# Kernel optimization log

Measured on AMD Instinct MI355X. Metric: run time of the kernel, lower is better.

## Reference

```python
import jax, jax.numpy as jnp
import numpy as np

HID = 1024
NH = 16
HD = HID // NH  # 64


def _lin_params(key, fan_in, fan_out):
    k1, k2 = jax.random.split(key)
    lim = 1.0 / np.sqrt(fan_in)
    W = jax.random.uniform(k1, (fan_in, fan_out), jnp.float32, -lim, lim)
    b = jax.random.uniform(k2, (fan_out,), jnp.float32, -lim, lim)
    return W, b


def setup_inputs() -> dict:
    key = jax.random.key(0)
    ks = jax.random.split(key, 12)
    B, S = 4, 1024
    inp = {
        'query': jax.random.normal(ks[0], (B, S, HID), jnp.float32),
        'key': jax.random.normal(ks[1], (B, S, HID), jnp.float32),
        'value': jax.random.normal(ks[2], (B, S, HID), jnp.float32),
    }
    inp['Wq'], inp['bq'] = _lin_params(ks[3], HID, HID)
    inp['Wk'], inp['bk'] = _lin_params(ks[4], HID, HID)
    inp['Wv'], inp['bv'] = _lin_params(ks[5], HID, HID)
    inp['Wp'], inp['bp'] = _lin_params(ks[6], HID, HID)
    inp['Wup'], inp['bup'] = _lin_params(ks[7], HD, 1)
    inp['Wud'], inp['bud'] = _lin_params(ks[8], HD, 1)
    inp['Wus'], inp['bus'] = _lin_params(ks[9], HID, NH)
    inp['Wo'], inp['bo'] = _lin_params(ks[10], HID, HID)
    return inp


def _split_heads(x, B, S):
    # [B,S,HID] -> [B,NH,S,HD]
    return x.reshape(B, S, NH, HD).transpose(0, 2, 1, 3)


def reference(query, key, value, Wq, bq, Wk, bk, Wv, bv, Wp, bp,
              Wup, bup, Wud, bud, Wus, bus, Wo, bo):
    B, S, _ = query.shape
    len_q = S

    q = query @ Wq + bq   # [B,S,HID]
    k = key @ Wk + bk
    v = value @ Wv + bv

    # Gaussian-window positional bias (per head, per query position)
    p = _split_heads(q @ Wp + bp, B, S)              # [B,NH,S,HD]
    tp = jnp.tanh(p)
    p_i = tp @ Wup + bup                             # [B,NH,S,1]
    z_i = tp @ Wud + bud                             # [B,NH,S,1]
    cen_pos = len_q * jax.nn.sigmoid(p_i)            # [B,NH,S,1]
    win_size = len_q * jax.nn.sigmoid(z_i)           # [B,NH,S,1]
    pos = jnp.arange(len_q, dtype=q.dtype)[None, None, None, :]  # [1,1,1,S]
    bias = (pos - cen_pos) ** 2 / (0.5 * win_size ** 2)          # [B,NH,S,S]

    # per-head alpha gate from raw query
    alpha = jax.nn.sigmoid(query @ Wus + bus)        # [B,S,NH]
    alpha = alpha.reshape(B, S, NH, 1).transpose(0, 2, 1, 3)  # [B,NH,S,1]

    qh = _split_heads(q, B, S)
    kh = _split_heads(k, B, S)
    vh = _split_heads(v, B, S)

    scale = 1.0 / jnp.sqrt(jnp.asarray(HD, q.dtype))
    scores = jnp.einsum('bhqd,bhkd->bhqk', qh, kh) * scale
    scores = scores - alpha * bias                   # inject gated Gaussian bias
    attn = jax.nn.softmax(scores, axis=-1)           # [B,NH,S,S]

    out = jnp.einsum('bhqk,bhkd->bhqd', attn, vh)    # [B,NH,S,HD]
    x = out.transpose(0, 2, 1, 3).reshape(B, S, HID)
    x = x @ Wo + bo
    return x, attn
```

## Files before the change

### kernel.cpp

```cpp
#include <hip/hip_runtime.h>
#include <hip/hip_bf16.h>
#include <math.h>

#define S_LEN 1024
#define HIDN  1024
#define NHEAD 16
#define HDIM  64
#define BATCH 4
#define MTOT  (BATCH * S_LEN)

typedef __attribute__((ext_vector_type(8))) short          bf16v8;
typedef __attribute__((ext_vector_type(8))) unsigned short u16v8;
typedef __attribute__((ext_vector_type(4))) unsigned short u16v4;
typedef __attribute__((ext_vector_type(4))) float          f32v4;

__device__ __forceinline__ unsigned short f2bf_rne(float x) {
    unsigned int u = __float_as_uint(x);
    unsigned int r = (u + 0x7fffu + ((u >> 16) & 1u)) >> 16;
    return (unsigned short)r;
}
__device__ __forceinline__ float bf2f(unsigned short h) {
    return __uint_as_float(((unsigned int)h) << 16);
}
__device__ __forceinline__ void split2(float x, unsigned short& h, unsigned short& l) {
    h = f2bf_rne(x);
    l = f2bf_rne(x - bf2f(h));
}

__global__ __launch_bounds__(256) void split_w4(
    const float* __restrict__ W0, const float* __restrict__ W1,
    const float* __restrict__ W2, const float* __restrict__ W3,
    unsigned short* __restrict__ Hbase, unsigned short* __restrict__ Lbase)
{
    __shared__ float T[64][65];
    const int t  = threadIdx.x;
    const int k0 = blockIdx.y * 64;
    const int n0 = blockIdx.x * 64;
    const int z  = blockIdx.z;
    const float* W = (z == 0) ? W0 : (z == 1) ? W1 : (z == 2) ? W2 : W3;
    unsigned short* H = Hbase + (size_t)z * 1024 * 1024;
    unsigned short* L = Lbase + (size_t)z * 1024 * 1024;

    const int r = t >> 4;
    const int c = (t & 15) * 4;
#pragma unroll
    for (int i = 0; i < 4; ++i) {
        const int rr = r + i * 16;
        const float4 v = *(const float4*)&W[(size_t)(k0 + rr) * 1024 + n0 + c];
        T[rr][c + 0] = v.x; T[rr][c + 1] = v.y;
        T[rr][c + 2] = v.z; T[rr][c + 3] = v.w;
    }
    __syncthreads();

    const int n  = t >> 2;
    const int ko = (t & 3) * 16;
    u16v8 h0, h1, l0, l1;
#pragma unroll
    for (int kk = 0; kk < 8; ++kk) {
        unsigned short hh, ll;
        split2(T[ko + kk][n], hh, ll);
        h0[kk] = hh; l0[kk] = ll;
    }
#pragma unroll
    for (int kk = 0; kk < 8; ++kk) {
        unsigned short hh, ll;
        split2(T[ko + 8 + kk][n], hh, ll);
        h1[kk] = hh; l1[kk] = ll;
    }
    unsigned short* Hp = &H[(size_t)(n0 + n) * 1024 + k0 + ko];
    unsigned short* Lp = &L[(size_t)(n0 + n) * 1024 + k0 + ko];
    *(u16v8*)(Hp)     = h0;
    *(u16v8*)(Hp + 8) = h1;
    *(u16v8*)(Lp)     = l0;
    *(u16v8*)(Lp + 8) = l1;
}

__global__ __launch_bounds__(256) void alpha_kernel(
    const float* __restrict__ X, const float* __restrict__ Wus,
    const float* __restrict__ bus, float* __restrict__ alpha)
{
    __shared__ float Ws[1024 * 16];
    const int t = threadIdx.x;
#pragma unroll
    for (int i = 0; i < 16; ++i) {
        const int idx = t + i * 256;
        *reinterpret_cast<float4*>(&Ws[idx * 4]) =
            *reinterpret_cast<const float4*>(&Wus[idx * 4]);
    }
    __syncthreads();

    const int r = t >> 4, c = t & 15;
    const size_t row = (size_t)blockIdx.x * 16 + r;
    const float* x = &X[row * 1024];
    float acc = 0.f;
    for (int kk = 0; kk < 1024; kk += 4) {
        const float4 xv = *reinterpret_cast<const float4*>(&x[kk]);
        acc = fmaf(xv.x, Ws[(kk + 0) * 16 + c], acc);
        acc = fmaf(xv.y, Ws[(kk + 1) * 16 + c], acc);
        acc = fmaf(xv.z, Ws[(kk + 2) * 16 + c], acc);
        acc = fmaf(xv.w, Ws[(kk + 3) * 16 + c], acc);
    }
    acc += bus[c];
    alpha[row * 16 + c] = 1.f / (1.f + expf(-acc));
}

template<int AF32, int EPI>
__global__ __launch_bounds__(512, 2) void gemm_t(
    const float* __restrict__ Af,
    const unsigned short* __restrict__ Ah, const unsigned short* __restrict__ Al,
    const unsigned short* __restrict__ Bh, const unsigned short* __restrict__ Bl,
    const float* __restrict__ bias, float* __restrict__ Cf,
    unsigned short* __restrict__ Ch, unsigned short* __restrict__ Cl,
    const float* __restrict__ Wup, const float* __restrict__ Wud,
    const float* __restrict__ bup, const float* __restrict__ bud,
    const float* __restrict__ alpha, float* __restrict__ cenp,
    float* __restrict__ c0p)
{
    __shared__ short Ash[128][72];
    __shared__ short Asl[128][72];
    __shared__ short Bsh[64][72];
    __shared__ short Bsl[64][72];
    __shared__ float PSUP[2][128], PSUD[2][128];

    const int t    = threadIdx.x;
    const int bm   = blockIdx.y * 128;
    const int bn   = blockIdx.x * 64;
    const int lane = t & 63;
    const int wid  = t >> 6;
    const int wr   = wid >> 1;
    const int wc   = wid & 1;
    const int fr   = lane & 15;
    const int fq   = lane >> 4;

    f32v4 zero = {0.f, 0.f, 0.f, 0.f};
    f32v4 acc[2][2];
#pragma unroll
    for (int i = 0; i < 2; ++i)
#pragma unroll
        for (int j = 0; j < 2; ++j) acc[i][j] = zero;

    const int sra = t >> 2;
    const int sca = (t & 3) * 16;
    const int tb  = t & 255;
    const int srb = tb >> 2;
    const int scb = (tb & 3) * 16;
    const bool isBl = (t >= 256);
    const unsigned short* pB = isBl ? &Bl[(size_t)(bn + srb) * 1024 + scb]
                                    : &Bh[(size_t)(bn + srb) * 1024 + scb];
    const float* pAf = AF32 ? &Af[(size_t)(bm + sra) * 1024 + sca] : nullptr;
    const unsigned short* pAh = AF32 ? nullptr : &Ah[(size_t)(bm + sra) * 1024 + sca];
    const unsigned short* pAl = AF32 ? nullptr : &Al[(size_t)(bm + sra) * 1024 + sca];

    u16v8 rah0, rah1, ral0, ral1, rb0, rb1;
    auto LOAD = [&](int k0) {
        if (AF32) {
            const float4 a0 = *(const float4*)(pAf + k0);
            const float4 a1 = *(const float4*)(pAf + k0 + 4);
            const float4 a2 = *(const float4*)(pAf + k0 + 8);
            const float4 a3 = *(const float4*)(pAf + k0 + 12);
            const float xs[16] = {a0.x, a0.y, a0.z, a0.w, a1.x, a1.y, a1.z, a1.w,
                                  a2.x, a2.y, a2.z, a2.w, a3.x, a3.y, a3.z, a3.w};
#pragma unroll
            for (int e = 0; e < 8; ++e) {
                unsigned short hh, ll;
                split2(xs[e], hh, ll);
                rah0[e] = hh; ral0[e] = ll;
            }
#pragma unroll
            for (int e = 0; e < 8; ++e) {
                unsigned short hh, ll;
                split2(xs[8 + e], hh, ll);
                rah1[e] = hh; ral1[e] = ll;
            }
        } else {
            rah0 = *(const u16v8*)(pAh + k0);
            rah1 = *(const u16v8*)(pAh + k0 + 8);
            ral0 = *(const u16v8*)(pAl + k0);
            ral1 = *(const u16v8*)(pAl + k0 + 8);
        }
        rb0 = *(const u16v8*)(pB + k0);
        rb1 = *(const u16v8*)(pB + k0 + 8);
    };

    LOAD(0);
    for (int k0 = 0; k0 < 1024; k0 += 64) {
        __syncthreads();
        *(u16v8*)&Ash[sra][sca]     = rah0;
        *(u16v8*)&Ash[sra][sca + 8] = rah1;
        *(u16v8*)&Asl[sra][sca]     = ral0;
        *(u16v8*)&Asl[sra][sca + 8] = ral1;
        if (isBl) {
            *(u16v8*)&Bsl[srb][scb]     = rb0;
            *(u16v8*)&Bsl[srb][scb + 8] = rb1;
        } else {
            *(u16v8*)&Bsh[srb][scb]     = rb0;
            *(u16v8*)&Bsh[srb][scb + 8] = rb1;
        }
        __syncthreads();

        if (k0 + 64 < 1024) LOAD(k0 + 64);

#pragma unroll
        for (int kk2 = 0; kk2 < 2; ++kk2) {
            const int ks = kk2 * 32 + fq * 8;
            bf16v8 fah[2], fal[2], fbh[2], fbl[2];
#pragma unroll
            for (int i = 0; i < 2; ++i) {
                fah[i] = *(const bf16v8*)&Ash[wr * 32 + i * 16 + fr][ks];
                fal[i] = *(const bf16v8*)&Asl[wr * 32 + i * 16 + fr][ks];
            }
#pragma unroll
            for (int j = 0; j < 2; ++j) {
                fbh[j] = *(const bf16v8*)&Bsh[wc * 32 + j * 16 + fr][ks];
                fbl[j] = *(const bf16v8*)&Bsl[wc * 32 + j * 16 + fr][ks];
            }
#pragma unroll
            for (int i = 0; i < 2; ++i)
#pragma unroll
                for (int j = 0; j < 2; ++j) {
                    acc[i][j] = __builtin_amdgcn_mfma_f32_16x16x32_bf16(
                        fah[i], fbh[j], acc[i][j], 0, 0, 0);
                    acc[i][j] = __builtin_amdgcn_mfma_f32_16x16x32_bf16(
                        fah[i], fbl[j], acc[i][j], 0, 0, 0);
                    acc[i][j] = __builtin_amdgcn_mfma_f32_16x16x32_bf16(
                        fal[i], fbh[j], acc[i][j], 0, 0, 0);
                }
        }
    }

    if (EPI == 3) {
        float wupj[2], wudj[2], bb[2];
#pragma unroll
        for (int j = 0; j < 2; ++j) {
            const int colL = wc * 32 + j * 16 + fr;
            wupj[j] = Wup[colL];
            wudj[j] = Wud[colL];
            bb[j]   = bias[bn + colL];
        }
        float su[2][4], sd[2][4];
#pragma unroll
        for (int i = 0; i < 2; ++i)
#pragma unroll
            for (int r = 0; r < 4; ++r) { su[i][r] = 0.f; sd[i][r] = 0.f; }
#pragma unroll
        for (int j = 0; j < 2; ++j)
#pragma unroll
            for (int i = 0; i < 2; ++i)
#pragma unroll
                for (int r = 0; r < 4; ++r) {
                    const float tv = tanhf(acc[i][j][r] + bb[j]);
                    su[i][r] = fmaf(tv, wupj[j], su[i][r]);
                    sd[i][r] = fmaf(tv, wudj[j], sd[i][r]);
                }
#pragma unroll
        for (int i = 0; i < 2; ++i)
#pragma unroll
            for (int r = 0; r < 4; ++r) {
                float a = su[i][r], d = sd[i][r];
                a += __shfl_xor(a, 1); d += __shfl_xor(d, 1);
                a += __shfl_xor(a, 2); d += __shfl_xor(d, 2);
                a += __shfl_xor(a, 4); d += __shfl_xor(d, 4);
                a += __shfl_xor(a, 8); d += __shfl_xor(d, 8);
                if (fr == 0) {
                    const int row = wr * 32 + i * 16 + fq * 4 + r;
                    PSUP[wc][row] = a;
                    PSUD[wc][row] = d;
                }
            }
        __syncthreads();
        if (t < 128) {
            const float ap = PSUP[0][t] + PSUP[1][t] + bup[0];
            const float az = PSUD[0][t] + PSUD[1][t] + bud[0];
            const float cenv = 1024.f / (1.f + expf(-ap));
            const float win  = 1024.f / (1.f + expf(-az));
            const int grow = bm + t;
            const int hd   = bn >> 6;
            const int zz   = (grow >> 10) * 16 + hd;
            const int s    = grow & 1023;
            const float al = alpha[(size_t)grow * 16 + hd];
            cenp[(size_t)zz * 1024 + s] = cenv;
            c0p[(size_t)zz * 1024 + s]  = al * 2.f / (win * win);
        }
        return;
    }

#pragma unroll
    for (int j = 0; j < 2; ++j) {
        const int col = bn + wc * 32 + j * 16 + fr;
        const float bb = bias[col];
#pragma unroll
        for (int i = 0; i < 2; ++i) {
            const int row0 = bm + wr * 32 + i * 16 + fq * 4;
            const f32v4 cv = acc[i][j];
            if (EPI == 2) {
                u16v4 h4, l4;
#pragma unroll
                for (int r = 0; r < 4; ++r) {
                    unsigned short hh, ll;
                    split2(cv[r] + bb, hh, ll);
                    h4[r] = hh; l4[r] = ll;
                }
                const size_t base =
                    ((size_t)((row0 >> 10) * 16 + (col >> 6)) * 64 + (col & 63)) * 1024
                    + (row0 & 1023);
                *(u16v4*)&Ch[base] = h4;
                *(u16v4*)&Cl[base] = l4;
            } else if (EPI == 1) {
#pragma unroll
                for (int r = 0; r < 4; ++r) {
                    unsigned short hh, ll;
                    split2(cv[r] + bb, hh, ll);
                    const size_t idx = (size_t)(row0 + r) * 1024 + col;
                    Ch[idx] = hh; Cl[idx] = ll;
                }
            } else {
#pragma unroll
                for (int r = 0; r < 4; ++r)
                    Cf[(size_t)(row0 + r) * 1024 + col] = cv[r] + bb;
            }
        }
    }
}

#define M0_SHIFT 8.0f
__global__ __launch_bounds__(512, 2) void attn_fused(
    const unsigned short* __restrict__ qh, const unsigned short* __restrict__ ql,
    const unsigned short* __restrict__ kh, const unsigned short* __restrict__ kl,
    const unsigned short* __restrict__ vTh, const unsigned short* __restrict__ vTl,
    const float* __restrict__ cen, const float* __restrict__ c0,
    float* __restrict__ attn,
    unsigned short* __restrict__ oh, unsigned short* __restrict__ ol)
{
    __shared__ unsigned short KH[64][64], KL[64][64];
    __shared__ unsigned short VH[64][64], VL[64][64];
    __shared__ unsigned short PH[128][64], PL[128][64];
    __shared__ float CEN[128], C0S[128];
    __shared__ float LSUM[2][128];
    __shared__ float RINV[128];

    const int bid   = blockIdx.x;
    const int z     = ((bid >> 6) << 3) | (bid & 7);
    const int itile = (bid >> 3) & 7;
    const int i0    = itile * 128;
    const int bq    = z >> 4;
    const int hd    = z & 15;

    const int t    = threadIdx.x;
    const int lane = t & 63;
    const int wid  = t >> 6;
    const int wrp  = wid >> 1;
    const int wc   = wid & 1;
    const int fr   = lane & 15, fq = lane >> 4;

    if (t < 128) {
        CEN[t] = cen[(size_t)z * 1024 + i0 + t];
        C0S[t] = c0[(size_t)z * 1024 + i0 + t];
    }

    bf16v8 qfh_[2][2], qfl_[2][2];
#pragma unroll
    for (int i = 0; i < 2; ++i)
#pragma unroll
        for (int kk = 0; kk < 2; ++kk) {
            const size_t qa = (size_t)(bq * 1024 + i0 + wrp * 32 + i * 16 + fr) * 1024
                              + hd * 64 + kk * 32 + fq * 8;
            qfh_[i][kk] = *(const bf16v8*)&qh[qa];
            qfl_[i][kk] = *(const bf16v8*)&ql[qa];
        }

    float lsum[2][4];
#pragma unroll
    for (int i = 0; i < 2; ++i)
#pragma unroll
        for (int r = 0; r < 4; ++r) lsum[i][r] = 0.f;

    const f32v4 zero = {0.f, 0.f, 0.f, 0.f};

    const int srow = t >> 3;
    const int sseg = t & 7;
    const int ssl  = (sseg ^ (srow & 7)) * 8;
    const unsigned short* vhb = vTh + (size_t)z * 64 * 1024;
    const unsigned short* vlb = vTl + (size_t)z * 64 * 1024;

    u16v8 rkh, rkl, rvh, rvl;
    auto LOADK = [&](int j0) {
        const size_t ga = (size_t)(bq * 1024 + j0 + srow) * 1024 + hd * 64 + sseg * 8;
        rkh = *(const u16v8*)&kh[ga];
        rkl = *(const u16v8*)&kl[ga];
    };
    auto LOADV = [&](int j0) {
        const size_t va = (size_t)srow * 1024 + j0 + sseg * 8;
        rvh = *(const u16v8*)&vhb[va];
        rvl = *(const u16v8*)&vlb[va];
    };

    LOADK(0);
    for (int jt = 0; jt < 16; ++jt) {
        const int j0 = jt * 64;
        unsigned short (*KHc)[64] = (jt & 1) ? VH : KH;
        unsigned short (*KLc)[64] = (jt & 1) ? VL : KL;
        *(u16v8*)&KHc[srow][ssl] = rkh;
        *(u16v8*)&KLc[srow][ssl] = rkl;
        __syncthreads();
        if (jt < 15) LOADK(j0 + 64);

        f32v4 acc[2][2];
#pragma unroll
        for (int i = 0; i < 2; ++i)
#pragma unroll
            for (int j2 = 0; j2 < 2; ++j2) acc[i][j2] = zero;

        __builtin_amdgcn_s_setprio(1);
#pragma unroll
        for (int kk = 0; kk < 2; ++kk) {
            bf16v8 fbh[2], fbl[2];
#pragma unroll
            for (int j2 = 0; j2 < 2; ++j2) {
                const int rb = wc * 32 + j2 * 16 + fr;
                const int sb = ((kk * 4 + fq) ^ (rb & 7)) * 8;
                fbh[j2] = *(const bf16v8*)&KHc[rb][sb];
                fbl[j2] = *(const bf16v8*)&KLc[rb][sb];
            }
#pragma unroll
            for (int i = 0; i < 2; ++i)
#pragma unroll
                for (int j2 = 0; j2 < 2; ++j2) {
                    acc[i][j2] = __builtin_amdgcn_mfma_f32_16x16x32_bf16(
                        qfh_[i][kk], fbh[j2], acc[i][j2], 0, 0, 0);
                    acc[i][j2] = __builtin_amdgcn_mfma_f32_16x16x32_bf16(
                        qfh_[i][kk], fbl[j2], acc[i][j2], 0, 0, 0);
                    acc[i][j2] = __builtin_amdgcn_mfma_f32_16x16x32_bf16(
                        qfl_[i][kk], fbh[j2], acc[i][j2], 0, 0, 0);
                }
        }
        __builtin_amdgcn_s_setprio(0);

#pragma unroll
        for (int i = 0; i < 2; ++i)
#pragma unroll
            for (int r = 0; r < 4; ++r) {
                const int row = wrp * 32 + i * 16 + fq * 4 + r;
                const float cv = CEN[row], cc = C0S[row];
                float al = 0.f;
#pragma unroll
                for (int j2 = 0; j2 < 2; ++j2) {
                    const int col = wc * 32 + j2 * 16 + fr;
                    const float dd = (float)(j0 + col) - cv;
                    const float s  = acc[i][j2][r] * 0.125f - cc * dd * dd;
                    al += __expf(s - M0_SHIFT);
                }
                lsum[i][r] += al;
            }
    }

#pragma unroll
    for (int i = 0; i < 2; ++i)
#pragma unroll
        for (int r = 0; r < 4; ++r) {
            float v = lsum[i][r];
            v += __shfl_xor(v, 1);
            v += __shfl_xor(v, 2);
            v += __shfl_xor(v, 4);
            v += __shfl_xor(v, 8);
            if (fr == 0) LSUM[wc][wrp * 32 + i * 16 + fq * 4 + r] = v;
        }
    __syncthreads();
    if (t < 128) RINV[t] = 1.f / (LSUM[0][t] + LSUM[1][t]);

    f32v4 acco[2][4];
#pragma unroll
    for (int i = 0; i < 2; ++i)
#pragma unroll
        for (int j = 0; j < 4; ++j) acco[i][j] = zero;

    float* attnZ = attn + (size_t)z * 1024 * 1024;

    LOADK(0);
    LOADV(0);
    for (int jt = 0; jt < 16; ++jt) {
        const int j0 = jt * 64;
        __syncthreads();
        *(u16v8*)&KH[srow][ssl] = rkh;
        *(u16v8*)&KL[srow][ssl] = rkl;
        *(u16v8*)&VH[srow][ssl] = rvh;
        *(u16v8*)&VL[srow][ssl] = rvl;
        __syncthreads();
        if (jt < 15) { LOADK(j0 + 64); LOADV(j0 + 64); }

        f32v4 acc[2][2];
#pragma unroll
        for (int i = 0; i < 2; ++i)
#pragma unroll
            for (int j2 = 0; j2 < 2; ++j2) acc[i][j2] = zero;

        __builtin_amdgcn_s_setprio(1);
#pragma unroll
        for (int kk = 0; kk < 2; ++kk) {
            bf16v8 fbh[2], fbl[2];
#pragma unroll
            for (int j2 = 0; j2 < 2; ++j2) {
                const int rb = wc * 32 + j2 * 16 + fr;
                const int sb = ((kk * 4 + fq) ^ (rb & 7)) * 8;
                fbh[j2] = *(const bf16v8*)&KH[rb][sb];
                fbl[j2] = *(const bf16v8*)&KL[rb][sb];
            }
#pragma unroll
            for (int i = 0; i < 2; ++i)
#pragma unroll
                for (int j2 = 0; j2 < 2; ++j2) {
                    acc[i][j2] = __builtin_amdgcn_mfma_f32_16x16x32_bf16(
                        qfh_[i][kk], fbh[j2], acc[i][j2], 0, 0, 0);
                    acc[i][j2] = __builtin_amdgcn_mfma_f32_16x16x32_bf16(
                        qfh_[i][kk], fbl[j2], acc[i][j2], 0, 0, 0);
                    acc[i][j2] = __builtin_amdgcn_mfma_f32_16x16x32_bf16(
                        qfl_[i][kk], fbh[j2], acc[i][j2], 0, 0, 0);
                }
        }
        __builtin_amdgcn_s_setprio(0);

#pragma unroll
        for (int i = 0; i < 2; ++i)
#pragma unroll
            for (int r = 0; r < 4; ++r) {
                const int row = wrp * 32 + i * 16 + fq * 4 + r;
                const float cv = CEN[row], cc = C0S[row], ri = RINV[row];
#pragma unroll
                for (int j2 = 0; j2 < 2; ++j2) {
                    const int col = wc * 32 + j2 * 16 + fr;
                    const float dd = (float)(j0 + col) - cv;
                    const float s  = acc[i][j2][r] * 0.125f - cc * dd * dd;
                    const float p  = __expf(s - M0_SHIFT) * ri;
                    attnZ[(size_t)(i0 + row) * 1024 + j0 + col] = p;
                    unsigned short hv, lv;
                    split2(p, hv, lv);
                    const int slot = ((col >> 3) ^ (row & 7)) * 8 + (col & 7);
                    PH[row][slot] = hv;
                    PL[row][slot] = lv;
                }
            }

        __builtin_amdgcn_s_setprio(1);
        {
            bf16v8 pah[2], pal[2];
#pragma unroll
            for (int iq = 0; iq < 2; ++iq) {
                const int rp = wrp * 32 + iq * 16 + fr;
                const int sp = ((wc * 4 + fq) ^ (rp & 7)) * 8;
                pah[iq] = *(const bf16v8*)&PH[rp][sp];
                pal[iq] = *(const bf16v8*)&PL[rp][sp];
            }
#pragma unroll
            for (int jd = 0; jd < 4; ++jd) {
                const int rb = jd * 16 + fr;
                const int sb = ((wc * 4 + fq) ^ (rb & 7)) * 8;
                const bf16v8 vfh = *(const bf16v8*)&VH[rb][sb];
                const bf16v8 vfl = *(const bf16v8*)&VL[rb][sb];
#pragma unroll
                for (int iq = 0; iq < 2; ++iq) {
                    acco[iq][jd] = __builtin_amdgcn_mfma_f32_16x16x32_bf16(
                        pah[iq], vfh, acco[iq][jd], 0, 0, 0);
                    acco[iq][jd] = __builtin_amdgcn_mfma_f32_16x16x32_bf16(
                        pah[iq], vfl, acco[iq][jd], 0, 0, 0);
                    acco[iq][jd] = __builtin_amdgcn_mfma_f32_16x16x32_bf16(
                        pal[iq], vfh, acco[iq][jd], 0, 0, 0);
                }
            }
        }
        __builtin_amdgcn_s_setprio(0);
    }

    __syncthreads();
    if (wc == 1) {
        float* s0 = (float*)PH;
        float* s1 = (float*)PL;
#pragma unroll
        for (int jd = 0; jd < 4; ++jd)
#pragma unroll
            for (int r = 0; r < 4; ++r) {
                const int idx = ((wrp * 4 + jd) * 4 + r) * 64 + lane;
                s0[idx] = acco[0][jd][r];
                s1[idx] = acco[1][jd][r];
            }
    }
    __syncthreads();
    if (wc == 0) {
        const float* s0 = (const float*)PH;
        const float* s1 = (const float*)PL;
#pragma unroll
        for (int jd = 0; jd < 4; ++jd) {
            const int dcol = jd * 16 + fr;
#pragma unroll
            for (int iq = 0; iq < 2; ++iq) {
                const int row0 = i0 + wrp * 32 + iq * 16 + fq * 4;
                const float* sp = (iq == 0) ? s0 : s1;
#pragma unroll
                for (int r = 0; r < 4; ++r) {
                    const float v = acco[iq][jd][r] +
                        sp[((wrp * 4 + jd) * 4 + r) * 64 + lane];
                    unsigned short hv, lv;
                    split2(v, hv, lv);
                    const size_t idx = (size_t)(bq * 1024 + row0 + r) * 1024
                                       + hd * 64 + dcol;
                    oh[idx] = hv;
                    ol[idx] = lv;
                }
            }
        }
    }
}

extern "C" void kernel_launch(void* const* d_in, const int* in_sizes, int n_in,
                              void* d_out, int out_size, void* d_ws, size_t ws_size,
                              hipStream_t stream)
{
    const float* query = (const float*)d_in[0];
    const float* key_  = (const float*)d_in[1];
    const float* value = (const float*)d_in[2];
    const float* Wq  = (const float*)d_in[3];
    const float* bq  = (const float*)d_in[4];
    const float* Wk  = (const float*)d_in[5];
    const float* bk  = (const float*)d_in[6];
    const float* Wv  = (const float*)d_in[7];
    const float* bv  = (const float*)d_in[8];
    const float* Wp  = (const float*)d_in[9];
    const float* bp  = (const float*)d_in[10];
    const float* Wup = (const float*)d_in[11];
    const float* bup = (const float*)d_in[12];
    const float* Wud = (const float*)d_in[13];
    const float* bud = (const float*)d_in[14];
    const float* Wus = (const float*)d_in[15];
    const float* bus = (const float*)d_in[16];
    const float* Wo  = (const float*)d_in[17];
    const float* bo  = (const float*)d_in[18];

    float* x_out = (float*)d_out;
    float* attn  = x_out + (size_t)MTOT * HIDN;

    char* wsb = (char*)d_ws;
    unsigned short* qh  = (unsigned short*)(wsb);
    unsigned short* ql  = (unsigned short*)(wsb + (8u  << 20));
    unsigned short* kh  = (unsigned short*)(wsb + (16u << 20));
    unsigned short* kl  = (unsigned short*)(wsb + (24u << 20));
    unsigned short* vTh = (unsigned short*)(wsb + (32u << 20));
    unsigned short* vTl = (unsigned short*)(wsb + (40u << 20));
    unsigned short* oh  = (unsigned short*)(wsb + (48u << 20));
    unsigned short* ol  = (unsigned short*)(wsb + (56u << 20));
    float* alpha_ws = (float*)(wsb + (64u << 20));
    float* cen_ws   = (float*)(wsb + (64u << 20) + (256u << 10));
    float* c0_ws    = (float*)(wsb + (64u << 20) + (512u << 10));
    unsigned short* wh = (unsigned short*)attn;
    unsigned short* wl = wh + (size_t)4 * 1024 * 1024;
    unsigned short* w2h = qh;
    unsigned short* w2l = ql;

    const dim3 blk(256);
    const dim3 blk512(512);
    const dim3 ggemm(HIDN / 64, MTOT / 128);
    const size_t WSTEP = (size_t)1024 * 1024;

    split_w4<<<dim3(16, 16, 4), blk, 0, stream>>>(Wq, Wk, Wv, Wp, wh, wl);
    alpha_kernel<<<dim3(MTOT / 16), blk, 0, stream>>>(query, Wus, bus, alpha_ws);
    gemm_t<1, 1><<<ggemm, blk512, 0, stream>>>(
        query, nullptr, nullptr, wh, wl, bq, nullptr, qh, ql,
        nullptr, nullptr, nullptr, nullptr, nullptr, nullptr, nullptr);
    gemm_t<1, 1><<<ggemm, blk512, 0, stream>>>(
        key_, nullptr, nullptr, wh + WSTEP, wl + WSTEP, bk, nullptr, kh, kl,
        nullptr, nullptr, nullptr, nullptr, nullptr, nullptr, nullptr);
    gemm_t<1, 2><<<ggemm, blk512, 0, stream>>>(
        value, nullptr, nullptr, wh + 2 * WSTEP, wl + 2 * WSTEP, bv,
        nullptr, vTh, vTl,
        nullptr, nullptr, nullptr, nullptr, nullptr, nullptr, nullptr);
    gemm_t<0, 3><<<ggemm, blk512, 0, stream>>>(
        nullptr, qh, ql, wh + 3 * WSTEP, wl + 3 * WSTEP, bp, nullptr,
        nullptr, nullptr,
        Wup, Wud, bup, bud, alpha_ws, cen_ws, c0_ws);
    attn_fused<<<dim3(512), blk512, 0, stream>>>(
        qh, ql, kh, kl, vTh, vTl, cen_ws, c0_ws, attn, oh, ol);
    split_w4<<<dim3(16, 16, 1), blk, 0, stream>>>(Wo, Wo, Wo, Wo, w2h, w2l);
    gemm_t<0, 0><<<ggemm, blk512, 0, stream>>>(
        nullptr, oh, ol, w2h, w2l, bo, x_out, nullptr, nullptr,
        nullptr, nullptr, nullptr, nullptr, nullptr, nullptr, nullptr);
}
```

Before: 368.2 us.

## Load K/V MFMA fragments directly from global memory instead of LDS staging

Removes the shared-memory staging of K and V tiles in both passes of the fused attention kernel. Each wave now reads its bf16 hi/lo MFMA operand fragments straight from global memory, relying on the cache. This drops the per-tile LDS writes, the register prefetch and the block-wide barriers. In exchange, the four wave-rows redundantly fetch the same K/V data, the loads are row-strided rather than coalesced, and global-load latency is no longer hidden by a software prefetch. The setprio scopes are narrowed to just the MFMA groups.

```diff
diff --git a/kernel.cpp b/kernel.cpp
--- a/kernel.cpp
+++ b/kernel.cpp
@@ -331,8 +331,6 @@
     float* __restrict__ attn,
     unsigned short* __restrict__ oh, unsigned short* __restrict__ ol)
 {
-    __shared__ unsigned short KH[64][64], KL[64][64];
-    __shared__ unsigned short VH[64][64], VL[64][64];
     __shared__ unsigned short PH[128][64], PL[128][64];
     __shared__ float CEN[128], C0S[128];
     __shared__ float LSUM[2][128];
@@ -376,33 +374,14 @@
 
     const f32v4 zero = {0.f, 0.f, 0.f, 0.f};
 
-    const int srow = t >> 3;
-    const int sseg = t & 7;
-    const int ssl  = (sseg ^ (srow & 7)) * 8;
+    const size_t kfbase = (size_t)(bq * 1024 + wc * 32 + fr) * 1024 + hd * 64 + fq * 8;
     const unsigned short* vhb = vTh + (size_t)z * 64 * 1024;
     const unsigned short* vlb = vTl + (size_t)z * 64 * 1024;
 
-    u16v8 rkh, rkl, rvh, rvl;
-    auto LOADK = [&](int j0) {
-        const size_t ga = (size_t)(bq * 1024 + j0 + srow) * 1024 + hd * 64 + sseg * 8;
-        rkh = *(const u16v8*)&kh[ga];
-        rkl = *(const u16v8*)&kl[ga];
-    };
-    auto LOADV = [&](int j0) {
-        const size_t va = (size_t)srow * 1024 + j0 + sseg * 8;
-        rvh = *(const u16v8*)&vhb[va];
-        rvl = *(const u16v8*)&vlb[va];
-    };
-
-    LOADK(0);
+    __syncthreads();
+
     for (int jt = 0; jt < 16; ++jt) {
         const int j0 = jt * 64;
-        unsigned short (*KHc)[64] = (jt & 1) ? VH : KH;
-        unsigned short (*KLc)[64] = (jt & 1) ? VL : KL;
-        *(u16v8*)&KHc[srow][ssl] = rkh;
-        *(u16v8*)&KLc[srow][ssl] = rkl;
-        __syncthreads();
-        if (jt < 15) LOADK(j0 + 64);
 
         f32v4 acc[2][2];
 #pragma unroll
@@ -410,17 +389,16 @@
 #pragma unroll
             for (int j2 = 0; j2 < 2; ++j2) acc[i][j2] = zero;
 
-        __builtin_amdgcn_s_setprio(1);
 #pragma unroll
         for (int kk = 0; kk < 2; ++kk) {
             bf16v8 fbh[2], fbl[2];
 #pragma unroll
             for (int j2 = 0; j2 < 2; ++j2) {
-                const int rb = wc * 32 + j2 * 16 + fr;
-                const int sb = ((kk * 4 + fq) ^ (rb & 7)) * 8;
-                fbh[j2] = *(const bf16v8*)&KHc[rb][sb];
-                fbl[j2] = *(const bf16v8*)&KLc[rb][sb];
-            }
+                const size_t ka = kfbase + ((size_t)j0 + j2 * 16) * 1024 + kk * 32;
+                fbh[j2] = *(const bf16v8*)&kh[ka];
+                fbl[j2] = *(const bf16v8*)&kl[ka];
+            }
+            __builtin_amdgcn_s_setprio(1);
 #pragma unroll
             for (int i = 0; i < 2; ++i)
 #pragma unroll
@@ -432,8 +410,8 @@
                     acc[i][j2] = __builtin_amdgcn_mfma_f32_16x16x32_bf16(
                         qfl_[i][kk], fbh[j2], acc[i][j2], 0, 0, 0);
                 }
-        }
-        __builtin_amdgcn_s_setprio(0);
+            __builtin_amdgcn_s_setprio(0);
+        }
 
 #pragma unroll
         for (int i = 0; i < 2; ++i)
@@ -466,6 +444,7 @@
         }
     __syncthreads();
     if (t < 128) RINV[t] = 1.f / (LSUM[0][t] + LSUM[1][t]);
+    __syncthreads();
 
     f32v4 acco[2][4];
 #pragma unroll
@@ -474,18 +453,10 @@
         for (int j = 0; j < 4; ++j) acco[i][j] = zero;
 
     float* attnZ = attn + (size_t)z * 1024 * 1024;
-
-    LOADK(0);
-    LOADV(0);
+    const size_t vfbase = (size_t)fr * 1024 + wc * 32 + fq * 8;
+
     for (int jt = 0; jt < 16; ++jt) {
         const int j0 = jt * 64;
-        __syncthreads();
-        *(u16v8*)&KH[srow][ssl] = rkh;
-        *(u16v8*)&KL[srow][ssl] = rkl;
-        *(u16v8*)&VH[srow][ssl] = rvh;
-        *(u16v8*)&VL[srow][ssl] = rvl;
-        __syncthreads();
-        if (jt < 15) { LOADK(j0 + 64); LOADV(j0 + 64); }
 
         f32v4 acc[2][2];
 #pragma unroll
@@ -493,17 +464,16 @@
 #pragma unroll
             for (int j2 = 0; j2 < 2; ++j2) acc[i][j2] = zero;
 
-        __builtin_amdgcn_s_setprio(1);
 #pragma unroll
         for (int kk = 0; kk < 2; ++kk) {
             bf16v8 fbh[2], fbl[2];
 #pragma unroll
             for (int j2 = 0; j2 < 2; ++j2) {
-                const int rb = wc * 32 + j2 * 16 + fr;
-                const int sb = ((kk * 4 + fq) ^ (rb & 7)) * 8;
-                fbh[j2] = *(const bf16v8*)&KH[rb][sb];
-                fbl[j2] = *(const bf16v8*)&KL[rb][sb];
-            }
+                const size_t ka = kfbase + ((size_t)j0 + j2 * 16) * 1024 + kk * 32;
+                fbh[j2] = *(const bf16v8*)&kh[ka];
+                fbl[j2] = *(const bf16v8*)&kl[ka];
+            }
+            __builtin_amdgcn_s_setprio(1);
 #pragma unroll
             for (int i = 0; i < 2; ++i)
 #pragma unroll
@@ -515,8 +485,8 @@
                     acc[i][j2] = __builtin_amdgcn_mfma_f32_16x16x32_bf16(
                         qfl_[i][kk], fbh[j2], acc[i][j2], 0, 0, 0);
                 }
-        }
-        __builtin_amdgcn_s_setprio(0);
+            __builtin_amdgcn_s_setprio(0);
+        }
 
 #pragma unroll
         for (int i = 0; i < 2; ++i)
@@ -539,7 +509,6 @@
                 }
             }
 
-        __builtin_amdgcn_s_setprio(1);
         {
             bf16v8 pah[2], pal[2];
 #pragma unroll
@@ -551,10 +520,10 @@
             }
 #pragma unroll
             for (int jd = 0; jd < 4; ++jd) {
-                const int rb = jd * 16 + fr;
-                const int sb = ((wc * 4 + fq) ^ (rb & 7)) * 8;
-                const bf16v8 vfh = *(const bf16v8*)&VH[rb][sb];
-                const bf16v8 vfl = *(const bf16v8*)&VL[rb][sb];
+                const size_t va = vfbase + (size_t)(jd * 16) * 1024 + j0;
+                const bf16v8 vfh = *(const bf16v8*)&vhb[va];
+                const bf16v8 vfl = *(const bf16v8*)&vlb[va];
+                __builtin_amdgcn_s_setprio(1);
 #pragma unroll
                 for (int iq = 0; iq < 2; ++iq) {
                     acco[iq][jd] = __builtin_amdgcn_mfma_f32_16x16x32_bf16(
@@ -564,9 +533,9 @@
                     acco[iq][jd] = __builtin_amdgcn_mfma_f32_16x16x32_bf16(
                         pal[iq], vfh, acco[iq][jd], 0, 0, 0);
                 }
-            }
-        }
-        __builtin_amdgcn_s_setprio(0);
+                __builtin_amdgcn_s_setprio(0);
+            }
+        }
     }
 
     __syncthreads();
```

Result: slower. 442.8 us (+20.2%).
